# Optimization experiments

Measured on AMD Instinct MI355X. Metric: run time of the kernel, lower is better.

Reference implementation:

```python
import math
import jax, jax.numpy as jnp
import numpy as np

B, T, C = 256, 200, 512
H = 8
N_ATTN = 512
HEAD = N_ATTN // H          # 64
ROT = HEAD // 2             # 32 (rotary_ndims = head_size * 0.5)
MAXLEN = 200
ITEM_NUM = 100000


def setup_inputs() -> dict:
    key = jax.random.key(0)
    ks = jax.random.split(key, 16)
    s = 0.02
    item_emb = jax.random.normal(ks[0], (ITEM_NUM + 1, C), jnp.float32) * s
    item_emb = item_emb.at[0].set(0.0)  # padding_idx=0
    inp = {
        "user_ids": jax.random.randint(ks[1], (B,), 0, 10000),
        "log_seqs": jax.random.randint(ks[2], (B, T), 0, ITEM_NUM + 1),
        "pos_seqs": jax.random.randint(ks[3], (B, T), 0, ITEM_NUM + 1),
        "neg_seqs": jax.random.randint(ks[4], (B, T), 0, ITEM_NUM + 1),
        "item_emb": item_emb,
        "time_w": 1.0 + jax.random.normal(ks[5], (H, MAXLEN), jnp.float32) * 0.1,
        "time_alpha": 1.0 + jax.random.normal(ks[6], (H, 1, MAXLEN), jnp.float32) * 0.1,
        "time_beta": 1.0 + jax.random.normal(ks[7], (H, MAXLEN, 1), jnp.float32) * 0.1,
        "time_gamma": 1.0 + jax.random.normal(ks[8], (MAXLEN, 1), jnp.float32) * 0.1,
        "Wq": jax.random.normal(ks[9], (N_ATTN, C), jnp.float32) * s,
        "bq": jnp.zeros((N_ATTN,), jnp.float32),
        "Wk": jax.random.normal(ks[10], (N_ATTN, C), jnp.float32) * s,
        "bk": jnp.zeros((N_ATTN,), jnp.float32),
        "Wv": jax.random.normal(ks[11], (N_ATTN, C), jnp.float32) * s,
        "bv": jnp.zeros((N_ATTN,), jnp.float32),
        "Wmix": jax.random.normal(ks[12], (H, H), jnp.float32) * (1.0 / math.sqrt(H)),
        "Wo": jax.random.normal(ks[13], (C, N_ATTN), jnp.float32) * s,
        "bo": jnp.zeros((C,), jnp.float32),
    }
    return inp


def _rotate_half(x):
    x1, x2 = x[..., : x.shape[-1] // 2], x[..., x.shape[-1] // 2 :]
    return jnp.concatenate((-x2, x1), axis=-1)


def _mha_pro(x_items, time_w, time_alpha, time_beta, time_gamma,
             Wq, bq, Wk, bk, Wv, bv, Wmix, Wo, bo):
    # x_items: [B, T, C]
    TT = MAXLEN
    # Toeplitz time-decay matrix built exactly like the torch pad/tile/reshape trick
    w = jnp.pad(time_w, ((0, 0), (0, TT)))          # [H, 2TT]
    w = jnp.tile(w, (1, TT))                         # [H, 2TT*TT]
    w = w[:, :-TT].reshape(H, TT, 2 * TT - 1)        # [H, TT, 2TT-1]
    w = w[:, :, TT - 1 :]                            # [H, TT, TT]
    w = w[:, :T, :T] * time_alpha[:, :, :T] * time_beta[:, :T, :]  # [H, T, T]

    # time_shift: shift first half of channels down by one token
    half = C // 2
    shifted = jnp.pad(x_items[:, :, :half], ((0, 0), (1, 0), (0, 0)))[:, :-1]
    x = jnp.concatenate([shifted, x_items[:, :, half:]], axis=-1)  # [B, T, C]

    q = (x @ Wq.T + bq).reshape(B, T, H, HEAD).transpose(0, 2, 1, 3)  # [B,H,T,D]
    k = (x @ Wk.T + bk).reshape(B, T, H, HEAD).transpose(0, 2, 1, 3)
    v = (x @ Wv.T + bv).reshape(B, T, H, HEAD).transpose(0, 2, 1, 3)

    # partial rotary on first ROT dims
    q_rot, q_pass = q[..., :ROT], q[..., ROT:]
    k_rot, k_pass = k[..., :ROT], k[..., ROT:]
    inv_freq = 1.0 / (10000.0 ** (jnp.arange(0, ROT, 2, dtype=jnp.float32) / ROT))
    freqs = jnp.arange(T, dtype=jnp.float32)[:, None] * inv_freq[None, :]  # [T, ROT/2]
    emb = jnp.concatenate((freqs, freqs), axis=-1)   # [T, ROT]
    cos, sin = jnp.cos(emb), jnp.sin(emb)
    q_rot = q_rot * cos + _rotate_half(q_rot) * sin
    k_rot = k_rot * cos + _rotate_half(k_rot) * sin
    q = jnp.concatenate((q_rot, q_pass), axis=-1)
    k = jnp.concatenate((k_rot, k_pass), axis=-1)

    att = jnp.einsum('bhtd,bhsd->bhts', q, k) * (1.0 / math.sqrt(HEAD))
    causal = jnp.tril(jnp.ones((T, T), bool))
    att = jnp.where(causal, att, -jnp.inf)
    att = jax.nn.softmax(att, axis=-1)
    att = att * w                                   # learned time-decay mask
    att = jnp.einsum('hg,bgts->bhts', Wmix, att)    # 1x1 conv across heads

    out = jnp.einsum('bhts,bhsd->bhtd', att, v)
    out = out.transpose(0, 2, 1, 3).reshape(B, T, N_ATTN)
    out = (out @ Wo.T + bo) * time_gamma[:T, :]
    return out


def reference(user_ids, log_seqs, pos_seqs, neg_seqs, item_emb,
              time_w, time_alpha, time_beta, time_gamma,
              Wq, bq, Wk, bk, Wv, bv, Wmix, Wo, bo):
    x_items = item_emb[log_seqs]                    # [B, T, C]
    log_feats = _mha_pro(x_items, time_w, time_alpha, time_beta, time_gamma,
                         Wq, bq, Wk, bk, Wv, bv, Wmix, Wo, bo)
    pos_embs = item_emb[pos_seqs]
    neg_embs = item_emb[neg_seqs]
    pos_logits = log_feats * pos_embs               # [B, T, C] (as in source)
    neg_logits = (log_feats * neg_embs).sum(axis=-1)  # [B, T]
    return pos_logits, neg_logits
```

## Files before the change

### kernel.cpp

```cpp
#include <hip/hip_runtime.h>

#define B_    256
#define T_    200
#define C_    512
#define H_    8
#define HEAD_ 64
#define M_    (B_ * T_)
#define POS_OUT_ (M_ * C_)
#define QK_ROWS_ 208
#define VT_PAD_  224
#define P_PAD_   232

typedef __attribute__((ext_vector_type(8))) short bf16x8;
typedef __attribute__((ext_vector_type(8))) _Float16 f16x8;
typedef __attribute__((ext_vector_type(4))) _Float16 f16x4;
typedef __attribute__((ext_vector_type(2))) _Float16 f16x2;
typedef __attribute__((ext_vector_type(4))) float f32x4;

__device__ __forceinline__ void gload16(const void* g, void* l) {
    __builtin_amdgcn_global_load_lds(
        (const __attribute__((address_space(1))) unsigned int*)g,
        (__attribute__((address_space(3))) unsigned int*)l, 16, 0, 0);
}

__global__ __launch_bounds__(256) void gather_shift_k(
    const float* __restrict__ emb, const int* __restrict__ logs,
    _Float16* __restrict__ x)
{
    int bt = blockIdx.x;
    int t  = bt % T_;
    int tid = threadIdx.x;
    int c  = tid * 2;
    _Float16* xr = x + (size_t)bt * C_;
    if (c < 256) {
        if (t == 0) {
            *(f16x2*)(xr + c) = (f16x2){(_Float16)0.0f, (_Float16)0.0f};
        } else {
            int id_prev = logs[bt - 1];
            float2 v = *(const float2*)(emb + (size_t)id_prev * C_ + c);
            *(f16x2*)(xr + c) = (f16x2){(_Float16)v.x, (_Float16)v.y};
        }
    } else {
        int id_cur = logs[bt];
        float2 v = *(const float2*)(emb + (size_t)id_cur * C_ + c);
        *(f16x2*)(xr + c) = (f16x2){(_Float16)v.x, (_Float16)v.y};
    }
}

__global__ __launch_bounds__(256) void convert_w_k(
    const float* __restrict__ Wq, const float* __restrict__ Wk,
    const float* __restrict__ Wv, const float* __restrict__ Wo,
    _Float16* __restrict__ dst)
{
    int idx = blockIdx.x * 256 + threadIdx.x;
    int mat = idx >> 16;
    int off = (idx & 65535) << 2;
    const float* src = (mat == 0) ? Wq : (mat == 1) ? Wk : (mat == 2) ? Wv : Wo;
    float4 v = *(const float4*)(src + off);
    f16x4 o = { (_Float16)v.x, (_Float16)v.y, (_Float16)v.z, (_Float16)v.w };
    *(f16x4*)(dst + ((size_t)mat << 18) + off) = o;
}

__global__ __launch_bounds__(256) void zero_pads_k(
    _Float16* __restrict__ Qb, _Float16* __restrict__ Kb,
    _Float16* __restrict__ Vt)
{
    int bh = blockIdx.x;
    int tid = threadIdx.x;
    for (int idx = tid; idx < 8 * 64; idx += 256) {
        Qb[(size_t)bh * QK_ROWS_ * 64 + 200 * 64 + idx] = (_Float16)0.0f;
        Kb[(size_t)bh * QK_ROWS_ * 64 + 200 * 64 + idx] = (_Float16)0.0f;
    }
    for (int idx = tid; idx < 64 * (VT_PAD_ - 200); idx += 256) {
        int d = idx / (VT_PAD_ - 200), s = 200 + idx % (VT_PAD_ - 200);
        Vt[(size_t)bh * 64 * VT_PAD_ + (size_t)d * VT_PAD_ + s] = (_Float16)0.0f;
    }
}

__global__ __launch_bounds__(256) void gemm_qkv_k(
    const _Float16* __restrict__ xh,
    const _Float16* __restrict__ Wh,
    const float* __restrict__ bq, const float* __restrict__ bk, const float* __restrict__ bv,
    _Float16* __restrict__ Qb, _Float16* __restrict__ Kb,
    _Float16* __restrict__ Vt,
    int nmt)
{
    int n = blockIdx.x;
    int mt, v;
    if ((nmt & 7) == 0) { int q8 = n & 7, i = n >> 3; mt = (i / 12) * 8 + q8; v = i % 12; }
    else               { mt = n / 12; v = n % 12; }
    int which = v >> 2;
    int nt    = v & 3;
    int m0    = mt * 128;
    const _Float16* Wm = Wh + ((size_t)(which * 4 + nt) * 128) * 512;
    const float* bias = (which == 0) ? bq : (which == 1) ? bk : bv;

    __shared__ _Float16 As[3][128 * 32];
    __shared__ _Float16 Bs[3][128 * 32];

    int tid  = threadIdx.x;
    int w    = tid >> 6, lane = tid & 63;
    int quad = lane >> 4, l15 = lane & 15;
    int wm   = w >> 1,    wn  = w & 1;
    int srow = lane >> 2, scg = lane & 3;
    int scg_src = scg ^ ((srow >> 1) & 3);
    int rq = (l15 >> 1) & 3;

    auto stage = [&](int buf, int k0) {
#pragma unroll
        for (int rr = 0; rr < 2; ++rr) {
            int seg = rr * 4 + w;
            int row = seg * 16 + srow;
            gload16(xh + (size_t)(m0 + row) * 512 + k0 + scg_src * 8, As[buf] + seg * 512);
            gload16(Wm + (size_t)row * 512 + k0 + scg_src * 8, Bs[buf] + seg * 512);
        }
    };

    f32x4 acc[4][4];
#pragma unroll
    for (int m = 0; m < 4; ++m)
#pragma unroll
        for (int nn = 0; nn < 4; ++nn) acc[m][nn] = (f32x4){0.f, 0.f, 0.f, 0.f};

    stage(0, 0);
    stage(1, 32);
#pragma unroll
    for (int s = 0; s < 16; ++s) {
        if (s < 15) asm volatile("s_waitcnt vmcnt(4)" ::: "memory");
        else        asm volatile("s_waitcnt vmcnt(0)" ::: "memory");
        __builtin_amdgcn_s_barrier();
        __builtin_amdgcn_sched_barrier(0);
        const _Float16* Ab = As[s % 3];
        const _Float16* Bb = Bs[s % 3];
        f16x8 af[4], bf[4];
#pragma unroll
        for (int m = 0; m < 4; ++m)
            af[m] = *(const f16x8*)(Ab + (wm * 4 + m) * 512 + l15 * 32 + (quad ^ rq) * 8);
#pragma unroll
        for (int nn = 0; nn < 4; ++nn)
            bf[nn] = *(const f16x8*)(Bb + (wn * 4 + nn) * 512 + l15 * 32 + (quad ^ rq) * 8);
        if (s <= 13) stage((s + 2) % 3, (s + 2) * 32);
#pragma unroll
        for (int m = 0; m < 4; ++m)
#pragma unroll
            for (int nn = 0; nn < 4; ++nn)
                acc[m][nn] = __builtin_amdgcn_mfma_f32_16x16x32_f16(af[m], bf[nn], acc[m][nn], 0, 0, 0);
    }

    int h = nt * 2 + wn;
    if (which < 2) {
        _Float16* dst = (which == 0) ? Qb : Kb;
        float sc = (which == 0) ? 0.125f : 1.0f;
        float invf = powf(10000.0f, -(float)l15 / 16.0f);
#pragma unroll
        for (int m = 0; m < 4; ++m) {
#pragma unroll
            for (int r = 0; r < 4; ++r) {
                int row = m0 + wm * 64 + m * 16 + quad * 4 + r;
                int bl = row / T_, t = row % T_;
                float sn, cs;
                __sincosf((float)t * invf, &sn, &cs);
                size_t base = ((size_t)(bl * 8 + h) * QK_ROWS_ + t) * 64;
                float av = acc[m][0][r] + bias[h * 64 + l15];
                float bv2 = acc[m][1][r] + bias[h * 64 + 16 + l15];
                dst[base + l15]      = (_Float16)((av * cs - bv2 * sn) * sc);
                dst[base + 16 + l15] = (_Float16)((bv2 * cs + av * sn) * sc);
                dst[base + 32 + l15] = (_Float16)((acc[m][2][r] + bias[h * 64 + 32 + l15]) * sc);
                dst[base + 48 + l15] = (_Float16)((acc[m][3][r] + bias[h * 64 + 48 + l15]) * sc);
            }
        }
    } else {
#pragma unroll
        for (int nn = 0; nn < 4; ++nn) {
            int ch = nn * 16 + l15;
            float bval = bias[h * 64 + ch];
#pragma unroll
            for (int m = 0; m < 4; ++m) {
                int r0 = m0 + wm * 64 + m * 16 + quad * 4;
                int t0v = r0 % T_;
                if (t0v <= 196) {
                    int bl = r0 / T_;
                    f16x4 v4 = {(_Float16)(acc[m][nn][0] + bval),
                                (_Float16)(acc[m][nn][1] + bval),
                                (_Float16)(acc[m][nn][2] + bval),
                                (_Float16)(acc[m][nn][3] + bval)};
                    *(f16x4*)(Vt + ((size_t)(bl * 8 + h) * 64 + ch) * VT_PAD_ + t0v) = v4;
                } else {
#pragma unroll
                    for (int r = 0; r < 4; ++r) {
                        int rw = r0 + r;
                        int bl = rw / T_, s = rw % T_;
                        Vt[((size_t)(bl * 8 + h) * 64 + ch) * VT_PAD_ + s] = (_Float16)(acc[m][nn][r] + bval);
                    }
                }
            }
        }
    }
}

__global__ __launch_bounds__(512) void attn_fused_k(
    const _Float16* __restrict__ Qb, const _Float16* __restrict__ Kb,
    const _Float16* __restrict__ Vt,
    const float* __restrict__ tw, const float* __restrict__ ta,
    const float* __restrict__ tb, const float* __restrict__ wmix,
    _Float16* __restrict__ ao)
{
    int n    = blockIdx.x;
    int xcd  = n & 7, slot = n >> 3;
    int i_tile = slot % 13;
    int b      = (slot / 13) * 8 + xcd;

    int tid  = threadIdx.x;
    int wave = tid >> 6, lane = tid & 63;
    int quad = lane >> 4, l15 = lane & 15;
    int t0   = i_tile * 16;
    int nst  = i_tile + 1;
    int smax = nst * 16;

    __shared__ _Float16 Pt[8][16][P_PAD_];
    __shared__ _Float16 twl[8 * 200];
    __shared__ float mixs[64];

    for (int idx = tid; idx < 1600; idx += 512) twl[idx] = (_Float16)tw[idx];
    if (tid < 64) mixs[tid] = wmix[tid];
    if (nst & 1) {
        for (int idx = tid; idx < 8 * 16 * 16; idx += 512) {
            int g = idx >> 8, row = (idx >> 4) & 15, s = smax + (idx & 15);
            Pt[g][row][s] = (_Float16)0.0f;
        }
    }
    __syncthreads();

    {
        int g = wave;
        const _Float16* Qg = Qb + (size_t)(b * 8 + g) * QK_ROWS_ * 64;
        const _Float16* Kg = Kb + (size_t)(b * 8 + g) * QK_ROWS_ * 64;
        f16x8 a0 = *(const f16x8*)(Qg + (size_t)(t0 + l15) * 64 + quad * 8);
        f16x8 a1 = *(const f16x8*)(Qg + (size_t)(t0 + l15) * 64 + quad * 8 + 32);

        f32x4 sf[13];
#pragma unroll
        for (int st = 0; st < 13; ++st) if (st < nst) {
            f16x8 k0 = *(const f16x8*)(Kg + (size_t)(st * 16 + l15) * 64 + quad * 8);
            f16x8 k1 = *(const f16x8*)(Kg + (size_t)(st * 16 + l15) * 64 + quad * 8 + 32);
            f32x4 c = {0.f, 0.f, 0.f, 0.f};
            c = __builtin_amdgcn_mfma_f32_16x16x32_f16(a0, k0, c, 0, 0, 0);
            c = __builtin_amdgcn_mfma_f32_16x16x32_f16(a1, k1, c, 0, 0, 0);
            sf[st] = c;
        }
        float inv[4];
#pragma unroll
        for (int r = 0; r < 4; ++r) {
            int t = t0 + quad * 4 + r;
            float sum = 0.f;
#pragma unroll
            for (int st = 0; st < 13; ++st) {
                if (st < nst - 1) {
                    float e = __expf(sf[st][r]); sf[st][r] = e; sum += e;
                } else if (st == nst - 1) {
                    int s = t0 + l15;
                    float e = (s <= t) ? __expf(sf[st][r]) : 0.f;
                    sf[st][r] = e; sum += e;
                }
            }
            sum += __shfl_xor(sum, 1);
            sum += __shfl_xor(sum, 2);
            sum += __shfl_xor(sum, 4);
            sum += __shfl_xor(sum, 8);
            inv[r] = 1.0f / sum;
        }
        float tbr[4];
#pragma unroll
        for (int r = 0; r < 4; ++r)
            tbr[r] = tb[g * 200 + min(t0 + quad * 4 + r, 199)];
#pragma unroll
        for (int st = 0; st < 13; ++st) if (st < nst) {
            int s = st * 16 + l15;
            float tav = ta[g * 200 + min(s, 199)];
#pragma unroll
            for (int r = 0; r < 4; ++r) {
                int t = t0 + quad * 4 + r;
                int wi = min(max(199 - t + s, 0), 199);
                float val = sf[st][r] * inv[r] * ((float)twl[g * 200 + wi] * tav * tbr[r]);
                Pt[g][quad * 4 + r][s] = (_Float16)val;
            }
        }
    }
    __syncthreads();

    {
        f16x2 mx[64];
#pragma unroll
        for (int i = 0; i < 64; ++i) {
            _Float16 mh = (_Float16)mixs[i];
            mx[i] = (f16x2){mh, mh};
        }
        int nitems = smax << 3;
        for (int idx = tid; idx < nitems; idx += 512) {
            int tloc = idx & 15;
            int sp   = (idx >> 4) << 1;
            f16x2 pv[8];
#pragma unroll
            for (int g = 0; g < 8; ++g) pv[g] = *(const f16x2*)&Pt[g][tloc][sp];
#pragma unroll
            for (int ho = 0; ho < 8; ++ho) {
                f16x2 o = mx[ho * 8] * pv[0];
#pragma unroll
                for (int g = 1; g < 8; ++g) o += mx[ho * 8 + g] * pv[g];
                *(f16x2*)&Pt[ho][tloc][sp] = o;
            }
        }
    }
    __syncthreads();

    {
        int nk = (nst + 1) >> 1;
        int hda = wave;
        const _Float16* Vh = Vt + (size_t)(b * 8 + hda) * 64 * VT_PAD_;
        f32x4 c4[4];
#pragma unroll
        for (int n2 = 0; n2 < 4; ++n2) c4[n2] = (f32x4){0.f, 0.f, 0.f, 0.f};
#pragma unroll
        for (int ks = 0; ks < 7; ++ks) if (ks < nk) {
            f16x8 a = *(const f16x8*)(&Pt[hda][l15][ks * 32 + quad * 8]);
#pragma unroll
            for (int n2 = 0; n2 < 4; ++n2) {
                f16x8 bb = *(const f16x8*)(Vh + (size_t)(n2 * 16 + l15) * VT_PAD_ + ks * 32 + quad * 8);
                c4[n2] = __builtin_amdgcn_mfma_f32_16x16x32_f16(a, bb, c4[n2], 0, 0, 0);
            }
        }
#pragma unroll
        for (int n2 = 0; n2 < 4; ++n2)
#pragma unroll
            for (int r = 0; r < 4; ++r) {
                int t = t0 + quad * 4 + r;
                if (t < 200)
                    ao[((size_t)(b * T_ + t)) * 512 + hda * 64 + n2 * 16 + l15] = (_Float16)c4[n2][r];
            }
    }
}

__global__ __launch_bounds__(256) void gemm_out_k(
    const _Float16* __restrict__ Ah, const _Float16* __restrict__ Woh,
    const float* __restrict__ bo, const float* __restrict__ gamma,
    float* __restrict__ dst, int nmt)
{
    int n = blockIdx.x;
    int mt, nt;
    if ((nmt & 7) == 0) { int q8 = n & 7, i = n >> 3; mt = (i / 4) * 8 + q8; nt = i % 4; }
    else               { mt = n / 4; nt = n % 4; }
    int m0 = mt * 128;
    const _Float16* Wm = Woh + (size_t)nt * 128 * 512;

    __shared__ _Float16 As[3][128 * 32];
    __shared__ _Float16 Bs[3][128 * 32];

    int tid  = threadIdx.x;
    int w    = tid >> 6, lane = tid & 63;
    int quad = lane >> 4, l15 = lane & 15;
    int wm   = w >> 1,    wn  = w & 1;
    int srow = lane >> 2, scg = lane & 3;
    int scg_src = scg ^ ((srow >> 1) & 3);
    int rq = (l15 >> 1) & 3;

    auto stage = [&](int buf, int k0) {
#pragma unroll
        for (int rr = 0; rr < 2; ++rr) {
            int seg = rr * 4 + w;
            int row = seg * 16 + srow;
            gload16(Ah + (size_t)(m0 + row) * 512 + k0 + scg_src * 8, As[buf] + seg * 512);
            gload16(Wm + (size_t)row * 512 + k0 + scg_src * 8, Bs[buf] + seg * 512);
        }
    };

    f32x4 acc[4][4];
#pragma unroll
    for (int m = 0; m < 4; ++m)
#pragma unroll
        for (int nn = 0; nn < 4; ++nn) acc[m][nn] = (f32x4){0.f, 0.f, 0.f, 0.f};

    stage(0, 0);
    stage(1, 32);
#pragma unroll
    for (int s = 0; s < 16; ++s) {
        if (s < 15) asm volatile("s_waitcnt vmcnt(4)" ::: "memory");
        else        asm volatile("s_waitcnt vmcnt(0)" ::: "memory");
        __builtin_amdgcn_s_barrier();
        __builtin_amdgcn_sched_barrier(0);
        const _Float16* Ab = As[s % 3];
        const _Float16* Bb = Bs[s % 3];
        f16x8 af[4], bf[4];
#pragma unroll
        for (int m = 0; m < 4; ++m)
            af[m] = *(const f16x8*)(Ab + (wm * 4 + m) * 512 + l15 * 32 + (quad ^ rq) * 8);
#pragma unroll
        for (int nn = 0; nn < 4; ++nn)
            bf[nn] = *(const f16x8*)(Bb + (wn * 4 + nn) * 512 + l15 * 32 + (quad ^ rq) * 8);
        if (s <= 13) stage((s + 2) % 3, (s + 2) * 32);
#pragma unroll
        for (int m = 0; m < 4; ++m)
#pragma unroll
            for (int nn = 0; nn < 4; ++nn)
                acc[m][nn] = __builtin_amdgcn_mfma_f32_16x16x32_f16(af[m], bf[nn], acc[m][nn], 0, 0, 0);
    }

#pragma unroll
    for (int m = 0; m < 4; ++m)
#pragma unroll
        for (int nn = 0; nn < 4; ++nn)
#pragma unroll
            for (int r = 0; r < 4; ++r) {
                int row = m0 + wm * 64 + m * 16 + quad * 4 + r;
                int col = nt * 128 + wn * 64 + nn * 16 + l15;
                dst[(size_t)row * 512 + col] = (acc[m][nn][r] + bo[col]) * gamma[row % T_];
            }
}

__global__ __launch_bounds__(256) void logits_k(
    const float* __restrict__ lf, const float* __restrict__ emb,
    const int* __restrict__ pos, const int* __restrict__ neg,
    float* __restrict__ out, int bt0)
{
    int wid = threadIdx.x >> 6, lane = threadIdx.x & 63;
    int bt = blockIdx.x * 4 + wid;
    const float* l  = lf  + (size_t)bt * 512;
    const float* pe = emb + (size_t)pos[bt] * 512;
    const float* ne = emb + (size_t)neg[bt] * 512;
    float* po = out + (size_t)(bt0 + bt) * 512;
    float nacc = 0.f;
#pragma unroll
    for (int rep = 0; rep < 2; ++rep) {
        int i4 = (lane + rep * 64) * 4;
        float4 lv = *(const float4*)(l  + i4);
        float4 pv = *(const float4*)(pe + i4);
        float4 nv = *(const float4*)(ne + i4);
        float4 ov;
        ov.x = lv.x * pv.x; ov.y = lv.y * pv.y;
        ov.z = lv.z * pv.z; ov.w = lv.w * pv.w;
        *(float4*)(po + i4) = ov;
        nacc += lv.x * nv.x + lv.y * nv.y + lv.z * nv.z + lv.w * nv.w;
    }
#pragma unroll
    for (int off = 32; off >= 1; off >>= 1) nacc += __shfl_xor(nacc, off);
    if (lane == 0)
        out[(size_t)POS_OUT_ + bt0 + bt] = nacc;
}

extern "C" void kernel_launch(void* const* d_in, const int* in_sizes, int n_in,
                              void* d_out, int out_size, void* d_ws, size_t ws_size,
                              hipStream_t stream)
{
    const int* logs = (const int*)d_in[1];
    const int* pos  = (const int*)d_in[2];
    const int* neg  = (const int*)d_in[3];
    const float* emb = (const float*)d_in[4];
    const float* tw  = (const float*)d_in[5];
    const float* ta  = (const float*)d_in[6];
    const float* tb  = (const float*)d_in[7];
    const float* tg  = (const float*)d_in[8];
    const float* Wq  = (const float*)d_in[9];
    const float* bq  = (const float*)d_in[10];
    const float* Wk  = (const float*)d_in[11];
    const float* bk  = (const float*)d_in[12];
    const float* Wv  = (const float*)d_in[13];
    const float* bv  = (const float*)d_in[14];
    const float* wmix= (const float*)d_in[15];
    const float* Wo  = (const float*)d_in[16];
    const float* bo  = (const float*)d_in[17];

    const size_t PER_B = (size_t)T_ * C_ * 2
                       + (size_t)8 * QK_ROWS_ * 64 * 2
                       + (size_t)8 * QK_ROWS_ * 64 * 2
                       + (size_t)8 * 64 * VT_PAD_ * 2
                       + (size_t)T_ * C_ * 2
                       + (size_t)T_ * C_ * 4;
    const size_t SZ_WH = (size_t)4 * 512 * 512 * 2;

    int CB = (ws_size >= SZ_WH + PER_B * B_) ? B_ : 32;
    int nch = B_ / CB;
    int CM = CB * T_;
    int NMT = CM / 128;

    char* p = (char*)d_ws;
    _Float16*       Wh  = (_Float16*)p;  p += SZ_WH;
    _Float16*       xh  = (_Float16*)p;  p += (size_t)CM * C_ * 2;
    _Float16*       Qb  = (_Float16*)p;  p += (size_t)CB * 8 * QK_ROWS_ * 64 * 2;
    _Float16*       Kb  = (_Float16*)p;  p += (size_t)CB * 8 * QK_ROWS_ * 64 * 2;
    _Float16*       Vt  = (_Float16*)p;  p += (size_t)CB * 8 * 64 * VT_PAD_ * 2;
    _Float16*       aoh = (_Float16*)p;  p += (size_t)CM * C_ * 2;
    float*          lf  = (float*)p;

    convert_w_k<<<1024, 256, 0, stream>>>(Wq, Wk, Wv, Wo, Wh);
    zero_pads_k<<<CB * 8, 256, 0, stream>>>(Qb, Kb, Vt);

    for (int c = 0; c < nch; ++c) {
        int bt0 = c * CM;
        gather_shift_k<<<CM, 256, 0, stream>>>(emb, logs + bt0, xh);
        gemm_qkv_k<<<NMT * 12, 256, 0, stream>>>(xh, Wh, bq, bk, bv, Qb, Kb, Vt, NMT);
        attn_fused_k<<<13 * CB, 512, 0, stream>>>(Qb, Kb, Vt, tw, ta, tb, wmix, aoh);
        gemm_out_k<<<NMT * 4, 256, 0, stream>>>(aoh, Wh + (size_t)3 * 512 * 512, bo, tg, lf, NMT);
        logits_k<<<CM / 4, 256, 0, stream>>>(lf, emb, pos + bt0, neg + bt0, (float*)d_out, bt0);
    }
}
```

Baseline: 694.1 us.

## Precompute time-decay weight table and shrink attention LDS footprint

Adds a setup kernel that builds the full per-head [208x208] product of time_w, time_alpha and time_beta once per call. The attention kernel then reads one value per score instead of gathering and multiplying three parameters, and no longer stages time_w into shared memory. The P tile padding shrinks from 232 to 208 columns; the zero fill of the odd tail is replaced by masking out-of-range A fragments in the PV loop. s_setprio is raised around the MFMA loops. This trades index arithmetic and LDS for a 1.4 MB global table read per block and a smaller LDS footprint, which may allow higher occupancy.

```diff
diff --git a/kernel.cpp b/kernel.cpp
--- a/kernel.cpp
+++ b/kernel.cpp
@@ -9,9 +9,8 @@
 #define POS_OUT_ (M_ * C_)
 #define QK_ROWS_ 208
 #define VT_PAD_  224
-#define P_PAD_   232
-
-typedef __attribute__((ext_vector_type(8))) short bf16x8;
+#define P_PAD_   208
+
 typedef __attribute__((ext_vector_type(8))) _Float16 f16x8;
 typedef __attribute__((ext_vector_type(4))) _Float16 f16x4;
 typedef __attribute__((ext_vector_type(2))) _Float16 f16x2;
@@ -61,6 +60,19 @@
     *(f16x4*)(dst + ((size_t)mat << 18) + off) = o;
 }
 
+__global__ __launch_bounds__(256) void wtab_k(
+    const float* __restrict__ tw, const float* __restrict__ ta,
+    const float* __restrict__ tb, float* __restrict__ wtab)
+{
+    int idx = blockIdx.x * 256 + threadIdx.x;
+    int g   = idx / (208 * 208);
+    int rem = idx % (208 * 208);
+    int t = rem / 208, s = rem % 208;
+    int tt = min(t, 199), ss = min(s, 199);
+    int wi = min(max(199 - tt + ss, 0), 199);
+    wtab[idx] = tw[g * 200 + wi] * ta[g * 200 + ss] * tb[g * 200 + tt];
+}
+
 __global__ __launch_bounds__(256) void zero_pads_k(
     _Float16* __restrict__ Qb, _Float16* __restrict__ Kb,
     _Float16* __restrict__ Vt)
@@ -201,8 +213,8 @@
 __global__ __launch_bounds__(512) void attn_fused_k(
     const _Float16* __restrict__ Qb, const _Float16* __restrict__ Kb,
     const _Float16* __restrict__ Vt,
-    const float* __restrict__ tw, const float* __restrict__ ta,
-    const float* __restrict__ tb, const float* __restrict__ wmix,
+    const float* __restrict__ wtab,
+    const float* __restrict__ wmix,
     _Float16* __restrict__ ao)
 {
     int n    = blockIdx.x;
@@ -218,17 +230,9 @@
     int smax = nst * 16;
 
     __shared__ _Float16 Pt[8][16][P_PAD_];
-    __shared__ _Float16 twl[8 * 200];
     __shared__ float mixs[64];
 
-    for (int idx = tid; idx < 1600; idx += 512) twl[idx] = (_Float16)tw[idx];
     if (tid < 64) mixs[tid] = wmix[tid];
-    if (nst & 1) {
-        for (int idx = tid; idx < 8 * 16 * 16; idx += 512) {
-            int g = idx >> 8, row = (idx >> 4) & 15, s = smax + (idx & 15);
-            Pt[g][row][s] = (_Float16)0.0f;
-        }
-    }
     __syncthreads();
 
     {
@@ -239,6 +243,7 @@
         f16x8 a1 = *(const f16x8*)(Qg + (size_t)(t0 + l15) * 64 + quad * 8 + 32);
 
         f32x4 sf[13];
+        __builtin_amdgcn_s_setprio(1);
 #pragma unroll
         for (int st = 0; st < 13; ++st) if (st < nst) {
             f16x8 k0 = *(const f16x8*)(Kg + (size_t)(st * 16 + l15) * 64 + quad * 8);
@@ -248,6 +253,7 @@
             c = __builtin_amdgcn_mfma_f32_16x16x32_f16(a1, k1, c, 0, 0, 0);
             sf[st] = c;
         }
+        __builtin_amdgcn_s_setprio(0);
         float inv[4];
 #pragma unroll
         for (int r = 0; r < 4; ++r) {
@@ -269,20 +275,15 @@
             sum += __shfl_xor(sum, 8);
             inv[r] = 1.0f / sum;
         }
-        float tbr[4];
-#pragma unroll
-        for (int r = 0; r < 4; ++r)
-            tbr[r] = tb[g * 200 + min(t0 + quad * 4 + r, 199)];
+        const float* wg = wtab + ((size_t)g * 208 + t0) * 208;
 #pragma unroll
         for (int st = 0; st < 13; ++st) if (st < nst) {
             int s = st * 16 + l15;
-            float tav = ta[g * 200 + min(s, 199)];
 #pragma unroll
             for (int r = 0; r < 4; ++r) {
-                int t = t0 + quad * 4 + r;
-                int wi = min(max(199 - t + s, 0), 199);
-                float val = sf[st][r] * inv[r] * ((float)twl[g * 200 + wi] * tav * tbr[r]);
-                Pt[g][quad * 4 + r][s] = (_Float16)val;
+                int trow = quad * 4 + r;
+                float wv = wg[trow * 208 + s];
+                Pt[g][trow][s] = (_Float16)(sf[st][r] * inv[r] * wv);
             }
         }
     }
@@ -320,15 +321,24 @@
         f32x4 c4[4];
 #pragma unroll
         for (int n2 = 0; n2 < 4; ++n2) c4[n2] = (f32x4){0.f, 0.f, 0.f, 0.f};
+        __builtin_amdgcn_s_setprio(1);
 #pragma unroll
         for (int ks = 0; ks < 7; ++ks) if (ks < nk) {
-            f16x8 a = *(const f16x8*)(&Pt[hda][l15][ks * 32 + quad * 8]);
+            int cc = ks * 32 + quad * 8;
+            bool oob = cc >= smax;
+            int cl = oob ? 0 : cc;
+            f16x8 a = *(const f16x8*)(&Pt[hda][l15][cl]);
+            if (oob) {
+#pragma unroll
+                for (int j = 0; j < 8; ++j) a[j] = (_Float16)0.0f;
+            }
 #pragma unroll
             for (int n2 = 0; n2 < 4; ++n2) {
                 f16x8 bb = *(const f16x8*)(Vh + (size_t)(n2 * 16 + l15) * VT_PAD_ + ks * 32 + quad * 8);
                 c4[n2] = __builtin_amdgcn_mfma_f32_16x16x32_f16(a, bb, c4[n2], 0, 0, 0);
             }
         }
+        __builtin_amdgcn_s_setprio(0);
 #pragma unroll
         for (int n2 = 0; n2 < 4; ++n2)
 #pragma unroll
@@ -475,29 +485,32 @@
                        + (size_t)T_ * C_ * 2
                        + (size_t)T_ * C_ * 4;
     const size_t SZ_WH = (size_t)4 * 512 * 512 * 2;
-
-    int CB = (ws_size >= SZ_WH + PER_B * B_) ? B_ : 32;
+    const size_t SZ_WT = (size_t)8 * 208 * 208 * 4;
+
+    int CB = (ws_size >= SZ_WH + SZ_WT + PER_B * B_) ? B_ : 32;
     int nch = B_ / CB;
     int CM = CB * T_;
     int NMT = CM / 128;
 
     char* p = (char*)d_ws;
-    _Float16*       Wh  = (_Float16*)p;  p += SZ_WH;
-    _Float16*       xh  = (_Float16*)p;  p += (size_t)CM * C_ * 2;
-    _Float16*       Qb  = (_Float16*)p;  p += (size_t)CB * 8 * QK_ROWS_ * 64 * 2;
-    _Float16*       Kb  = (_Float16*)p;  p += (size_t)CB * 8 * QK_ROWS_ * 64 * 2;
-    _Float16*       Vt  = (_Float16*)p;  p += (size_t)CB * 8 * 64 * VT_PAD_ * 2;
-    _Float16*       aoh = (_Float16*)p;  p += (size_t)CM * C_ * 2;
-    float*          lf  = (float*)p;
+    _Float16*       Wh   = (_Float16*)p;  p += SZ_WH;
+    float*          wtab = (float*)p;     p += SZ_WT;
+    _Float16*       xh   = (_Float16*)p;  p += (size_t)CM * C_ * 2;
+    _Float16*       Qb   = (_Float16*)p;  p += (size_t)CB * 8 * QK_ROWS_ * 64 * 2;
+    _Float16*       Kb   = (_Float16*)p;  p += (size_t)CB * 8 * QK_ROWS_ * 64 * 2;
+    _Float16*       Vt   = (_Float16*)p;  p += (size_t)CB * 8 * 64 * VT_PAD_ * 2;
+    _Float16*       aoh  = (_Float16*)p;  p += (size_t)CM * C_ * 2;
+    float*          lf   = (float*)p;
 
     convert_w_k<<<1024, 256, 0, stream>>>(Wq, Wk, Wv, Wo, Wh);
+    wtab_k<<<1352, 256, 0, stream>>>(tw, ta, tb, wtab);
     zero_pads_k<<<CB * 8, 256, 0, stream>>>(Qb, Kb, Vt);
 
     for (int c = 0; c < nch; ++c) {
         int bt0 = c * CM;
         gather_shift_k<<<CM, 256, 0, stream>>>(emb, logs + bt0, xh);
         gemm_qkv_k<<<NMT * 12, 256, 0, stream>>>(xh, Wh, bq, bk, bv, Qb, Kb, Vt, NMT);
-        attn_fused_k<<<13 * CB, 512, 0, stream>>>(Qb, Kb, Vt, tw, ta, tb, wmix, aoh);
+        attn_fused_k<<<13 * CB, 512, 0, stream>>>(Qb, Kb, Vt, wtab, wmix, aoh);
         gemm_out_k<<<NMT * 4, 256, 0, stream>>>(aoh, Wh + (size_t)3 * 512 * 512, bo, tg, lf, NMT);
         logits_k<<<CM / 4, 256, 0, stream>>>(lf, emb, pos + bt0, neg + bt0, (float*)d_out, bt0);
     }
```

Measured after the change: 700.2 us. Within noise of the previous version (+0.9%).
